# Performance work log

Hardware: AMD Instinct MI355X
Metric: run time of the kernel (lower is better)

## Reference

```python
import jax, jax.numpy as jnp
import numpy as np
from jax import lax

DILS = [2 ** i for i in range(11)] * 3  # 33 layers


def _conv1(x, w, b):
    # kernel_size=1 conv: w (O,I), x (B,I,T)
    return jnp.einsum('oi,bit->bot', w, x) + b[None, :, None]


def _dconv2(x, w, b, d):
    # kernel_size=2 dilated conv, torch padding='same': pad (d//2, d-d//2)
    y = lax.conv_general_dilated(
        x, w, window_strides=(1,), padding=[(d // 2, d - d // 2)],
        rhs_dilation=(d,), dimension_numbers=('NCH', 'OIH', 'NCH'))
    return y + b[None, :, None]


def setup_inputs() -> dict:
    key = jax.random.key(0)
    ks = jax.random.split(key, 7)
    B, T = 32, 16384
    s1 = 1.0           # fan_in=1*1
    s16 = 1.0 / np.sqrt(16.0)
    s16k2 = 1.0 / np.sqrt(16.0 * 2)
    s32 = 1.0 / np.sqrt(32.0)
    return {
        'x': jax.random.normal(ks[0], (B, 1, T), jnp.float32),
        'w1_first': jax.random.normal(ks[1], (16, 1), jnp.float32) * s1,
        'b1_first': jnp.zeros((16,), jnp.float32),
        'w1_post': jax.random.normal(ks[2], (32, 16, 16), jnp.float32) * s16,
        'b1_post': jnp.zeros((32, 16), jnp.float32),
        'wf': jax.random.normal(ks[3], (33, 32, 16, 2), jnp.float32) * s16k2,
        'bf': jnp.zeros((33, 32), jnp.float32),
        'wg': jax.random.normal(ks[4], (33, 32, 16, 2), jnp.float32) * s16k2,
        'bg': jnp.zeros((33, 32), jnp.float32),
        'w2': jax.random.normal(ks[5], (33, 16, 32), jnp.float32) * s32,
        'b2': jnp.zeros((33, 16), jnp.float32),
    }


def reference(x, w1_first, b1_first, w1_post, b1_post, wf, bf, wg, bg, w2, b2):
    skip_sum = 0.0
    for i, d in enumerate(DILS):
        if i == 0:
            x = jax.nn.relu(_conv1(x, w1_first, b1_first))
        else:
            x = jax.nn.relu(_conv1(x, w1_post[i - 1], b1_post[i - 1]))
        x_f = _dconv2(x, wf[i], bf[i], d)
        x_g = _dconv2(x, wg[i], bg[i], d)
        z = jnp.tanh(x_f) * jax.nn.sigmoid(x_g)
        z = jax.nn.relu(_conv1(z, w2[i], b2[i]))
        x = x + z
        skip_sum = skip_sum + z
    return jax.nn.relu(skip_sum)
```

## Files before the change

kernel.cpp:

```cpp
#include <hip/hip_runtime.h>

#define BB 32
#define TT 16384

typedef __attribute__((ext_vector_type(8))) short bf16x8;
typedef __attribute__((ext_vector_type(4))) float f32x4;
typedef __attribute__((ext_vector_type(4))) int i32x4;

#define MFMA(A, B, C) __builtin_amdgcn_mfma_f32_16x16x32_bf16((A), (B), (C), 0, 0, 0)

__device__ __forceinline__ unsigned short bf16_rne(float f) {
    unsigned int u = __float_as_uint(f);
    return (unsigned short)((u + 0x7FFF + ((u >> 16) & 1)) >> 16);
}
__device__ __forceinline__ float bf16_to_f(unsigned short h) {
    return __uint_as_float(((unsigned int)h) << 16);
}
__device__ __forceinline__ uint2 pk4(f32x4 v) {
    uint2 r;
    asm("v_cvt_pk_bf16_f32 %0, %1, %2" : "=v"(r.x) : "v"(v[0]), "v"(v[1]));
    asm("v_cvt_pk_bf16_f32 %0, %1, %2" : "=v"(r.y) : "v"(v[2]), "v"(v[3]));
    return r;
}
__device__ __forceinline__ void split4(f32x4 v, uint2& hh, uint2& ll) {
    asm("v_cvt_pk_bf16_f32 %0, %1, %2" : "=v"(hh.x) : "v"(v[0]), "v"(v[1]));
    asm("v_cvt_pk_bf16_f32 %0, %1, %2" : "=v"(hh.y) : "v"(v[2]), "v"(v[3]));
    float l0 = v[0] - __uint_as_float(hh.x << 16);
    float l1 = v[1] - __uint_as_float(hh.x & 0xffff0000u);
    float l2 = v[2] - __uint_as_float(hh.y << 16);
    float l3 = v[3] - __uint_as_float(hh.y & 0xffff0000u);
    asm("v_cvt_pk_bf16_f32 %0, %1, %2" : "=v"(ll.x) : "v"(l0), "v"(l1));
    asm("v_cvt_pk_bf16_f32 %0, %1, %2" : "=v"(ll.y) : "v"(l2), "v"(l3));
}

__device__ __forceinline__ float fast_sigmoid(float x) {
    float e = __expf(-x);
    return __builtin_amdgcn_rcpf(1.0f + e);
}
__device__ __forceinline__ float fast_tanh(float x) {
    float ax = fabsf(x);
    float e = __expf(2.0f * ax);
    float r = 1.0f - 2.0f * __builtin_amdgcn_rcpf(1.0f + e);
    return copysignf(r, x);
}

__global__ void prep_kernel(const float* __restrict__ w1_first,
                            const float* __restrict__ b1_first,
                            const float* __restrict__ w1_post,
                            const float* __restrict__ b1_post,
                            const float* __restrict__ wf, const float* __restrict__ bfb,
                            const float* __restrict__ wg, const float* __restrict__ bgb,
                            const float* __restrict__ w2, const float* __restrict__ b2,
                            short* __restrict__ Wfrag, float* __restrict__ Bset) {
    int L = blockIdx.x;
    int l = threadIdx.x;
    int op = l & 15;
    int q = l >> 4;
    int i0 = (q & 1) << 3;
    int tap = q >> 1;

    float gbuf[6][8];
#pragma unroll
    for (int j = 0; j < 8; ++j) {
        gbuf[0][j] = (L == 0) ? 0.f
                   : w1_post[((size_t)(L - 1) * 16 + op) * 16 + i0 + j];
        gbuf[1][j] = wf[(((size_t)L * 32 + op) * 16 + i0 + j) * 2 + tap];
        gbuf[2][j] = wf[(((size_t)L * 32 + 16 + op) * 16 + i0 + j) * 2 + tap];
        gbuf[3][j] = wg[(((size_t)L * 32 + op) * 16 + i0 + j) * 2 + tap];
        gbuf[4][j] = wg[(((size_t)L * 32 + 16 + op) * 16 + i0 + j) * 2 + tap];
        gbuf[5][j] = w2[((size_t)L * 16 + op) * 32 + (q << 3) + j];
    }

    constexpr int gsel[7] = {0, 0, 1, 2, 3, 4, 5};
    constexpr int hsel[7] = {1, 0, 1, 1, 1, 1, 1};
#pragma unroll
    for (int f = 0; f < 7; ++f) {
        size_t base = (((size_t)L * 7 + f) * 64 + l) * 8;
#pragma unroll
        for (int j = 0; j < 8; ++j) {
            float v = gbuf[gsel[f]][j];
            unsigned short h = bf16_rne(v);
            Wfrag[base + j] = hsel[f] ? (short)h
                                      : (short)bf16_rne(v - bf16_to_f(h));
        }
    }

#pragma unroll
    for (int r = 0; r < 4; ++r) {
        int c = (q << 2) + r;
        float bv[6];
        bv[0] = (L == 0) ? b1_first[c] : b1_post[(size_t)(L - 1) * 16 + c];
        bv[1] = bfb[(size_t)L * 32 + c];
        bv[2] = bfb[(size_t)L * 32 + 16 + c];
        bv[3] = bgb[(size_t)L * 32 + c];
        bv[4] = bgb[(size_t)L * 32 + 16 + c];
        bv[5] = b2[(size_t)L * 16 + c];
#pragma unroll
        for (int s = 0; s < 6; ++s)
            Bset[(((size_t)L * 6 + s) * 64 + l) * 4 + r] = bv[s];
    }
}

__device__ __forceinline__ f32x4 conv1_eval(bool first, const void* __restrict__ xin,
                                            const float* __restrict__ w1f,
                                            int b, int tp, int q,
                                            f32x4 b1v, bf16x8 A1, bf16x8 A2) {
    const f32x4 zero = {0.f, 0.f, 0.f, 0.f};
    bool valid = ((unsigned)tp) < (unsigned)TT;
    f32x4 acc = valid ? b1v : zero;
    if (first) {
        const float* xf = (const float*)xin;
        float xv = valid ? xf[(size_t)b * TT + tp] : 0.f;
        const float4* w4 = (const float4*)w1f;
        float4 w = w4[q];
        acc[0] = fmaf(w.x, xv, acc[0]);
        acc[1] = fmaf(w.y, xv, acc[1]);
        acc[2] = fmaf(w.z, xv, acc[2]);
        acc[3] = fmaf(w.w, xv, acc[3]);
    } else {
        int tpc = valid ? tp : 0;
        const bf16x8 z8 = {0, 0, 0, 0, 0, 0, 0, 0};
        const bf16x8* xp = (const bf16x8*)((const char*)xin +
                            ((size_t)b * TT + tpc) * 64 + (q << 4));
        bf16x8 bb = valid ? *xp : z8;
        acc = MFMA(A1, bb, acc);
        acc = MFMA(A2, bb, acc);
    }
#pragma unroll
    for (int r = 0; r < 4; ++r) acc[r] = fmaxf(acc[r], 0.f);
    return acc;
}

template <int MODE>
__global__ __launch_bounds__(256) void wn_layer(
    const void* __restrict__ xin, void* __restrict__ xout,
    float* __restrict__ skip, float* __restrict__ dout,
    const short* __restrict__ WfragL, const float* __restrict__ BsetL,
    const float* __restrict__ w1f, int d) {
    __shared__ char sm[8192];

    const int tid = threadIdx.x;
    const int wave = tid >> 6, lane = tid & 63;
    const int p = lane & 15, q = lane >> 4;

    const int blk = ((blockIdx.x & 7) << 10) + (blockIdx.x >> 3);
    const int b = blk >> 8;
    const int tbase = ((blk & 255) << 6) + (wave << 4);
    const int pl = d >> 1, pr = d - pl;

    char* xrb = sm + wave * 1024;
    char* zb = sm + 4096 + wave * 1024;
    const int xorb = (p & 8) << 2;

    const bf16x8* WF = (const bf16x8*)WfragL;
    const f32x4* BS = (const f32x4*)BsetL;

    const f32x4 b1v = BS[lane];
    bf16x8 A1 = {0, 0, 0, 0, 0, 0, 0, 0};
    bf16x8 A2 = {0, 0, 0, 0, 0, 0, 0, 0};
    if (MODE != 1) { A1 = WF[lane]; A2 = WF[64 + lane]; }

#pragma unroll
    for (int g = 0; g < 2; ++g) {
        int ts = tbase + (g ? pr : -pl);
        f32x4 xr = conv1_eval(MODE == 1, xin, w1f, b, ts + p, q, b1v, A1, A2);
        *(uint2*)(xrb + (g << 9) +
                  ((((q >> 1) << 8) + (p << 4) + ((q & 1) << 3)) ^ xorb)) = pk4(xr);
    }

    f32x4 xrC = {0.f, 0.f, 0.f, 0.f};
    if (MODE != 2)
        xrC = conv1_eval(MODE == 1, xin, w1f, b, tbase + p, q, b1v, A1, A2);

    bf16x8 bxr = *(const bf16x8*)(xrb + ((q >> 1) << 9) +
                                  ((((q & 1) << 8) + (p << 4)) ^ xorb));
    f32x4 f0 = MFMA(WF[2 * 64 + lane], bxr, BS[64 + lane]);
    f32x4 f1 = MFMA(WF[3 * 64 + lane], bxr, BS[128 + lane]);
    f32x4 g0 = MFMA(WF[4 * 64 + lane], bxr, BS[192 + lane]);
    f32x4 g1 = MFMA(WF[5 * 64 + lane], bxr, BS[256 + lane]);

    f32x4 z0, z1;
#pragma unroll
    for (int r = 0; r < 4; ++r) {
        z0[r] = fast_tanh(f0[r]) * fast_sigmoid(g0[r]);
        z1[r] = fast_tanh(f1[r]) * fast_sigmoid(g1[r]);
    }
    {
        int base = (((q >> 1) << 8) + (p << 4) + ((q & 1) << 3)) ^ xorb;
        *(uint2*)(zb + base) = pk4(z0);
        *(uint2*)(zb + 512 + base) = pk4(z1);
    }

    bf16x8 bz = *(const bf16x8*)(zb + (((q << 8) + (p << 4)) ^ xorb));
    f32x4 z2 = MFMA(WF[6 * 64 + lane], bz, BS[320 + lane]);
#pragma unroll
    for (int r = 0; r < 4; ++r) z2[r] = fmaxf(z2[r], 0.f);

    size_t pos = (size_t)b * TT + tbase + p;
    size_t xidx = (pos << 4) + (q << 2);
    if (MODE != 2) {
        f32x4 xo;
#pragma unroll
        for (int r = 0; r < 4; ++r) xo[r] = xrC[r] + z2[r];
        uint2 hh, ll;
        split4(xo, hh, ll);
        char* xob = (char*)xout + pos * 64;
        *(uint2*)(xob + (q << 3)) = hh;
        *(uint2*)(xob + 32 + (q << 3)) = ll;
        if (MODE == 1) {
            *(f32x4*)(skip + xidx) = z2;
        } else {
            f32x4 s = *(const f32x4*)(skip + xidx);
#pragma unroll
            for (int r = 0; r < 4; ++r) s[r] += z2[r];
            *(f32x4*)(skip + xidx) = s;
        }
    } else {
        f32x4 s = *(const f32x4*)(skip + xidx);
        size_t ob = (size_t)b * (16 * (size_t)TT) + (size_t)(q << 2) * TT + (tbase + p);
#pragma unroll
        for (int r = 0; r < 4; ++r)
            dout[ob + (size_t)r * TT] = fmaxf(s[r] + z2[r], 0.f);
    }
}

__global__ __launch_bounds__(256, 2) void wn_fused(
    const char* __restrict__ Xin, char* __restrict__ Xout,
    float* __restrict__ skip,
    const short* __restrict__ Wfrag, const float* __restrict__ Bset,
    int Lbase, int d0p, int NL) {
    extern __shared__ char sm[];
    char* Abuf = sm;
    char* Ubuf = sm + 49152;

    const int tid = threadIdx.x;
    const int wave = tid >> 6, lane = tid & 63;
    const int p = lane & 15, q = lane >> 4;
    char* zb = sm + 73728 + wave * 1024;
    const int xorb = (p & 8) << 2;

    const int gblk = ((blockIdx.x & 7) << 7) | (blockIdx.x >> 3);
    const int b = gblk >> 5;
    const int gt0 = ((gblk & 31) << 9) - 128;

#pragma unroll
    for (int jj = 0; jj < 3; ++jj) {
        int pos = jj * 256 + tid;
        int g = gt0 + pos;
        bool valid = ((unsigned)g) < (unsigned)TT;
        const char* src = Xin + ((size_t)b * TT + (valid ? g : 0)) * 64;
#pragma unroll
        for (int sub = 0; sub < 4; ++sub) {
            i32x4 v = {0, 0, 0, 0};
            if (valid) v = *(const i32x4*)(src + sub * 16);
            *(i32x4*)(Abuf + sub * 12288 + pos * 16) = v;
        }
    }
    __syncthreads();

    int uLo = 0, uHi = 48;
    f32x4 sk[8];
#pragma unroll
    for (int m = 0; m < 8; ++m) sk[m] = f32x4{0.f, 0.f, 0.f, 0.f};

#pragma unroll 1
    for (int k = 0; k < NL; ++k) {
        const int L = Lbase + k;
        const int d = 1 << (d0p + k);
        const int pl = d >> 1, pr = d - pl;
        const int tl = (pl + 15) >> 4, tr = (pr + 15) >> 4;
        const bool lastk = (k == NL - 1);
        const int nLo = uLo + tl, nHi = uHi - tr;

        const bf16x8* WF = (const bf16x8*)(Wfrag + (size_t)L * 7 * 64 * 8);
        const f32x4* BS = (const f32x4*)(Bset + (size_t)L * 6 * 64 * 4);
        const bf16x8 A1 = WF[lane], A2 = WF[64 + lane];
        const bf16x8 Wf0 = WF[128 + lane], Wf1 = WF[192 + lane];
        const bf16x8 Wg0 = WF[256 + lane], Wg1 = WF[320 + lane];
        const bf16x8 W2f = WF[384 + lane];
        const f32x4 b1v = BS[lane];
        const f32x4 bf0 = BS[64 + lane], bf1 = BS[128 + lane];
        const f32x4 bg0 = BS[192 + lane], bg1 = BS[256 + lane];
        const f32x4 b2v = BS[320 + lane];

        f32x4 ureg[12];

#pragma unroll
        for (int m = 0; m < 12; ++m) {
            int T = 4 * m + wave;
            if (T >= uLo && T < uHi) {
                int pos = T * 16 + p;
                bf16x8 bb = *(const bf16x8*)(Abuf + q * 12288 + pos * 16);
                f32x4 acc = b1v;
                acc = MFMA(A1, bb, acc);
                acc = MFMA(A2, bb, acc);
                bool val = ((unsigned)(gt0 + pos)) < (unsigned)TT;
#pragma unroll
                for (int r = 0; r < 4; ++r)
                    acc[r] = val ? fmaxf(acc[r], 0.f) : 0.f;
                ureg[m] = acc;
                *(uint2*)(Ubuf + (q >> 1) * 12288 + pos * 16 + ((q & 1) << 3)) =
                    pk4(acc);
            }
        }
        __syncthreads();

#pragma unroll
        for (int m = 0; m < 12; ++m) {
            int T = 4 * m + wave;
            bool doit = lastk ? (m >= 2 && m <= 9) : (T >= nLo && T < nHi);
            if (doit) {
                int pos = T * 16 + p;
                int tap = (q >> 1) ? pr : -pl;
                bf16x8 bxr = *(const bf16x8*)(Ubuf + (q & 1) * 12288 + (pos + tap) * 16);
                f32x4 f0 = MFMA(Wf0, bxr, bf0);
                f32x4 f1 = MFMA(Wf1, bxr, bf1);
                f32x4 g0 = MFMA(Wg0, bxr, bg0);
                f32x4 g1 = MFMA(Wg1, bxr, bg1);

                f32x4 z0, z1;
#pragma unroll
                for (int r = 0; r < 4; ++r) {
                    z0[r] = fast_tanh(f0[r]) * fast_sigmoid(g0[r]);
                    z1[r] = fast_tanh(f1[r]) * fast_sigmoid(g1[r]);
                }
                int zbase = (((q >> 1) << 8) + (p << 4) + ((q & 1) << 3)) ^ xorb;
                *(uint2*)(zb + zbase) = pk4(z0);
                *(uint2*)(zb + 512 + zbase) = pk4(z1);
                bf16x8 bz = *(const bf16x8*)(zb + (((q << 8) + (p << 4)) ^ xorb));
                f32x4 z2 = MFMA(W2f, bz, b2v);
#pragma unroll
                for (int r = 0; r < 4; ++r) z2[r] = fmaxf(z2[r], 0.f);

                int g = gt0 + pos;
                f32x4 xo = ureg[m] + z2;

                uint2 hh, ll;
                split4(xo, hh, ll);
                if (!lastk) {
                    *(uint2*)(Abuf + (q >> 1) * 12288 + pos * 16 + ((q & 1) << 3)) = hh;
                    *(uint2*)(Abuf + (2 + (q >> 1)) * 12288 + pos * 16 + ((q & 1) << 3)) = ll;
                } else {
                    char* gx = Xout + ((size_t)b * TT + g) * 64;
                    *(uint2*)(gx + (q >> 1) * 16 + ((q & 1) << 3)) = hh;
                    *(uint2*)(gx + 32 + (q >> 1) * 16 + ((q & 1) << 3)) = ll;
                }
                if (m >= 2 && m <= 9) sk[m - 2] += z2;
            }
        }
        __syncthreads();
        uLo = nLo;
        uHi = nHi;
    }

#pragma unroll
    for (int m = 2; m <= 9; ++m) {
        int T = 4 * m + wave;
        int g = gt0 + T * 16 + p;
        float* sp = skip + (((size_t)b * TT + g) << 4) + (q << 2);
        f32x4 s = *(const f32x4*)sp;
#pragma unroll
        for (int r = 0; r < 4; ++r) s[r] += sk[m - 2][r];
        *(f32x4*)sp = s;
    }
}

extern "C" void kernel_launch(void* const* d_in, const int* in_sizes, int n_in,
                              void* d_out, int out_size, void* d_ws, size_t ws_size,
                              hipStream_t stream) {
    const float* x        = (const float*)d_in[0];
    const float* w1_first = (const float*)d_in[1];
    const float* b1_first = (const float*)d_in[2];
    const float* w1_post  = (const float*)d_in[3];
    const float* b1_post  = (const float*)d_in[4];
    const float* wf       = (const float*)d_in[5];
    const float* bf       = (const float*)d_in[6];
    const float* wg       = (const float*)d_in[7];
    const float* bg       = (const float*)d_in[8];
    const float* w2       = (const float*)d_in[9];
    const float* b2       = (const float*)d_in[10];

    void* X0 = d_ws;
    float* SK = (float*)((char*)d_ws + 33554432);
    short* Wfrag = (short*)((char*)d_ws + 67108864);
    float* Bset = (float*)((char*)d_ws + 67345408);
    void* XD = d_out;
    float* dout = (float*)d_out;

    static bool attr_done = false;
    if (!attr_done) {
        hipFuncSetAttribute(reinterpret_cast<const void*>(wn_fused),
                            hipFuncAttributeMaxDynamicSharedMemorySize, 77824);
        attr_done = true;
    }

    prep_kernel<<<33, 64, 0, stream>>>(w1_first, b1_first, w1_post, b1_post,
                                       wf, bf, wg, bg, w2, b2, Wfrag, Bset);

    dim3 sblock(256), sgrid(BB * TT / 64);
    dim3 fblock(256), fgrid(BB * TT / 512);

    int n = 0;
    const void* cur_in = (const void*)x;
    auto nxt = [&](int parity) -> void* { return (parity & 1) ? XD : X0; };

    {
        void* out = nxt(n);
        wn_layer<1><<<sgrid, sblock, 0, stream>>>(cur_in, out, SK, dout,
                                                  Wfrag, Bset, w1_first, 1);
        cur_in = out; n ^= 1;
    }
    for (int cyc = 0; cyc < 3; ++cyc) {
        int Lb = (cyc == 0) ? 1 : 11 * cyc;
        int d0p = (cyc == 0) ? 1 : 0;
        int NL = (cyc == 0) ? 6 : 7;
        {
            void* out = nxt(n);
            wn_fused<<<fgrid, fblock, 77824, stream>>>(
                (const char*)cur_in, (char*)out, SK, Wfrag, Bset, Lb, d0p, NL);
            cur_in = out; n ^= 1;
        }
        int Ls = Lb + NL;
        for (int L = Ls; L <= Ls + 3; ++L) {
            int d = 1 << (L % 11);
            const short* WfL = Wfrag + (size_t)L * 7 * 64 * 8;
            const float* BsL = Bset + (size_t)L * 6 * 64 * 4;
            if (L == 32) {
                wn_layer<2><<<sgrid, sblock, 0, stream>>>(cur_in, nullptr, SK, dout,
                                                          WfL, BsL, w1_first, d);
            } else {
                void* out = nxt(n);
                wn_layer<0><<<sgrid, sblock, 0, stream>>>(cur_in, out, SK, dout,
                                                          WfL, BsL, w1_first, d);
                cur_in = out; n ^= 1;
            }
        }
    }
}
```

Measured before the change: 737.9 us.

## Add smaller-tile fused multi-layer kernel to raise occupancy

Adds a variant of the fused multi-layer WaveNet kernel that works on a 512-position window (256 output positions plus halo) instead of 768. It needs 52 KB of shared memory and is launched on twice as many blocks, aiming for more resident blocks per CU and better latency hiding. The variant is chosen at runtime through an occupancy query and used only if at least three blocks fit per CU. The cost is a larger halo share: proportionally more redundant recomputation at the window edges and more input reads per output.

Measured after the change: 738.4 us. Within noise of the previous version (+0.1%).

```diff
diff --git a/kernel.cpp b/kernel.cpp
--- a/kernel.cpp
+++ b/kernel.cpp
@@ -365,6 +365,150 @@
     }
 }
 
+__global__ __launch_bounds__(256, 2) void wn_fused512(
+    const char* __restrict__ Xin, char* __restrict__ Xout,
+    float* __restrict__ skip,
+    const short* __restrict__ Wfrag, const float* __restrict__ Bset,
+    int Lbase, int d0p, int NL) {
+    extern __shared__ char sm[];
+    char* Abuf = sm;
+    char* Ubuf = sm + 32768;
+
+    const int tid = threadIdx.x;
+    const int wave = tid >> 6, lane = tid & 63;
+    const int p = lane & 15, q = lane >> 4;
+    char* zb = sm + 49152 + wave * 1024;
+    const int xorb = (p & 8) << 2;
+
+    const int gblk = ((blockIdx.x & 7) << 8) | (blockIdx.x >> 3);
+    const int b = gblk >> 6;
+    const int gt0 = ((gblk & 63) << 8) - 112;
+
+#pragma unroll
+    for (int jj = 0; jj < 2; ++jj) {
+        int pos = jj * 256 + tid;
+        int g = gt0 + pos;
+        bool valid = ((unsigned)g) < (unsigned)TT;
+        const char* src = Xin + ((size_t)b * TT + (valid ? g : 0)) * 64;
+#pragma unroll
+        for (int sub = 0; sub < 4; ++sub) {
+            i32x4 v = {0, 0, 0, 0};
+            if (valid) v = *(const i32x4*)(src + sub * 16);
+            *(i32x4*)(Abuf + sub * 8192 + pos * 16) = v;
+        }
+    }
+    __syncthreads();
+
+    int uLo = 0, uHi = 32;
+    f32x4 sk[8];
+#pragma unroll
+    for (int m = 0; m < 8; ++m) sk[m] = f32x4{0.f, 0.f, 0.f, 0.f};
+
+#pragma unroll 1
+    for (int k = 0; k < NL; ++k) {
+        const int L = Lbase + k;
+        const int d = 1 << (d0p + k);
+        const int pl = d >> 1, pr = d - pl;
+        const int tl = (pl + 15) >> 4, tr = (pr + 15) >> 4;
+        const bool lastk = (k == NL - 1);
+        const int nLo = uLo + tl, nHi = uHi - tr;
+
+        const bf16x8* WF = (const bf16x8*)(Wfrag + (size_t)L * 7 * 64 * 8);
+        const f32x4* BS = (const f32x4*)(Bset + (size_t)L * 6 * 64 * 4);
+        const bf16x8 A1 = WF[lane], A2 = WF[64 + lane];
+        const bf16x8 Wf0 = WF[128 + lane], Wf1 = WF[192 + lane];
+        const bf16x8 Wg0 = WF[256 + lane], Wg1 = WF[320 + lane];
+        const bf16x8 W2f = WF[384 + lane];
+        const f32x4 b1v = BS[lane];
+        const f32x4 bf0 = BS[64 + lane], bf1 = BS[128 + lane];
+        const f32x4 bg0 = BS[192 + lane], bg1 = BS[256 + lane];
+        const f32x4 b2v = BS[320 + lane];
+
+        f32x4 ureg[8];
+
+#pragma unroll
+        for (int m = 0; m < 8; ++m) {
+            int T = 4 * m + wave;
+            if (T >= uLo && T < uHi) {
+                int pos = T * 16 + p;
+                bf16x8 bb = *(const bf16x8*)(Abuf + q * 8192 + pos * 16);
+                f32x4 acc = b1v;
+                acc = MFMA(A1, bb, acc);
+                acc = MFMA(A2, bb, acc);
+                bool val = ((unsigned)(gt0 + pos)) < (unsigned)TT;
+#pragma unroll
+                for (int r = 0; r < 4; ++r)
+                    acc[r] = val ? fmaxf(acc[r], 0.f) : 0.f;
+                ureg[m] = acc;
+                *(uint2*)(Ubuf + (q >> 1) * 8192 + pos * 16 + ((q & 1) << 3)) =
+                    pk4(acc);
+            }
+        }
+        __syncthreads();
+
+#pragma unroll
+        for (int m = 0; m < 8; ++m) {
+            int T = 4 * m + wave;
+            bool outT = (T >= 7 && T < 23);
+            bool doit = lastk ? outT : (T >= nLo && T < nHi);
+            if (doit) {
+                int pos = T * 16 + p;
+                int tap = (q >> 1) ? pr : -pl;
+                bf16x8 bxr = *(const bf16x8*)(Ubuf + (q & 1) * 8192 + (pos + tap) * 16);
+                f32x4 f0 = MFMA(Wf0, bxr, bf0);
+                f32x4 f1 = MFMA(Wf1, bxr, bf1);
+                f32x4 g0 = MFMA(Wg0, bxr, bg0);
+                f32x4 g1 = MFMA(Wg1, bxr, bg1);
+
+                f32x4 z0, z1;
+#pragma unroll
+                for (int r = 0; r < 4; ++r) {
+                    z0[r] = fast_tanh(f0[r]) * fast_sigmoid(g0[r]);
+                    z1[r] = fast_tanh(f1[r]) * fast_sigmoid(g1[r]);
+                }
+                int zbase = (((q >> 1) << 8) + (p << 4) + ((q & 1) << 3)) ^ xorb;
+                *(uint2*)(zb + zbase) = pk4(z0);
+                *(uint2*)(zb + 512 + zbase) = pk4(z1);
+                bf16x8 bz = *(const bf16x8*)(zb + (((q << 8) + (p << 4)) ^ xorb));
+                f32x4 z2 = MFMA(W2f, bz, b2v);
+#pragma unroll
+                for (int r = 0; r < 4; ++r) z2[r] = fmaxf(z2[r], 0.f);
+
+                int g = gt0 + pos;
+                f32x4 xo = ureg[m] + z2;
+
+                uint2 hh, ll;
+                split4(xo, hh, ll);
+                if (!lastk) {
+                    *(uint2*)(Abuf + (q >> 1) * 8192 + pos * 16 + ((q & 1) << 3)) = hh;
+                    *(uint2*)(Abuf + (2 + (q >> 1)) * 8192 + pos * 16 + ((q & 1) << 3)) = ll;
+                } else {
+                    char* gx = Xout + ((size_t)b * TT + g) * 64;
+                    *(uint2*)(gx + (q >> 1) * 16 + ((q & 1) << 3)) = hh;
+                    *(uint2*)(gx + 32 + (q >> 1) * 16 + ((q & 1) << 3)) = ll;
+                }
+                if (outT) sk[m] += z2;
+            }
+        }
+        __syncthreads();
+        uLo = nLo;
+        uHi = nHi;
+    }
+
+#pragma unroll
+    for (int m = 0; m < 8; ++m) {
+        int T = 4 * m + wave;
+        if (T >= 7 && T < 23) {
+            int g = gt0 + T * 16 + p;
+            float* sp = skip + (((size_t)b * TT + g) << 4) + (q << 2);
+            f32x4 s = *(const f32x4*)sp;
+#pragma unroll
+            for (int r = 0; r < 4; ++r) s[r] += sk[m][r];
+            *(f32x4*)sp = s;
+        }
+    }
+}
+
 extern "C" void kernel_launch(void* const* d_in, const int* in_sizes, int n_in,
                               void* d_out, int out_size, void* d_ws, size_t ws_size,
                               hipStream_t stream) {
@@ -391,14 +535,23 @@
     if (!attr_done) {
         hipFuncSetAttribute(reinterpret_cast<const void*>(wn_fused),
                             hipFuncAttributeMaxDynamicSharedMemorySize, 77824);
+        hipFuncSetAttribute(reinterpret_cast<const void*>(wn_fused512),
+                            hipFuncAttributeMaxDynamicSharedMemorySize, 53248);
         attr_done = true;
     }
+
+    int blk512 = 0;
+    hipOccupancyMaxActiveBlocksPerMultiprocessor(
+        &blk512, reinterpret_cast<const void*>(wn_fused512), 256, 53248);
+    const bool use512 = (blk512 >= 3);
 
     prep_kernel<<<33, 64, 0, stream>>>(w1_first, b1_first, w1_post, b1_post,
                                        wf, bf, wg, bg, w2, b2, Wfrag, Bset);
 
     dim3 sblock(256), sgrid(BB * TT / 64);
-    dim3 fblock(256), fgrid(BB * TT / 512);
+    dim3 fblock(256);
+    dim3 fgrid768(BB * TT / 512);
+    dim3 fgrid512(BB * TT / 256);
 
     int n = 0;
     const void* cur_in = (const void*)x;
@@ -416,8 +569,13 @@
         int NL = (cyc == 0) ? 6 : 7;
         {
             void* out = nxt(n);
-            wn_fused<<<fgrid, fblock, 77824, stream>>>(
-                (const char*)cur_in, (char*)out, SK, Wfrag, Bset, Lb, d0p, NL);
+            if (use512) {
+                wn_fused512<<<fgrid512, fblock, 53248, stream>>>(
+                    (const char*)cur_in, (char*)out, SK, Wfrag, Bset, Lb, d0p, NL);
+            } else {
+                wn_fused<<<fgrid768, fblock, 77824, stream>>>(
+                    (const char*)cur_in, (char*)out, SK, Wfrag, Bset, Lb, d0p, NL);
+            }
             cur_in = out; n ^= 1;
         }
         int Ls = Lb + NL;
```

## Shrink fused tile to 256 outputs and keep only bf16-high inside fused layers

Applied to the files above, without the earlier changes.

The fused multi-layer kernel now handles 256 output timesteps per block with a 496-sample halo window instead of 512 with 768, so shared memory drops from about 76 KB to 35 KB and the grid doubles. Intermediate activations between fused layers are stored as a single bf16 value rather than a hi/lo bf16 pair, which lets the first 1x1 conv use one MFMA instead of two and halves LDS traffic. The intent is higher occupancy and less per-layer compute. The cost is proportionally more halo recompute per output and lower precision for intermediates, which may affect accuracy.

New measurement: 805.8 us. 1.09x slower.

```diff
diff --git a/kernel.cpp b/kernel.cpp
--- a/kernel.cpp
+++ b/kernel.cpp
@@ -224,41 +224,43 @@
     }
 }
 
-__global__ __launch_bounds__(256, 2) void wn_fused(
+__global__ __launch_bounds__(256, 2) void wn_fused496s(
     const char* __restrict__ Xin, char* __restrict__ Xout,
     float* __restrict__ skip,
     const short* __restrict__ Wfrag, const float* __restrict__ Bset,
     int Lbase, int d0p, int NL) {
     extern __shared__ char sm[];
     char* Abuf = sm;
-    char* Ubuf = sm + 49152;
+    char* Ubuf = sm + 15872;
 
     const int tid = threadIdx.x;
     const int wave = tid >> 6, lane = tid & 63;
     const int p = lane & 15, q = lane >> 4;
-    char* zb = sm + 73728 + wave * 1024;
+    char* zb = sm + 31744 + wave * 1024;
     const int xorb = (p & 8) << 2;
 
-    const int gblk = ((blockIdx.x & 7) << 7) | (blockIdx.x >> 3);
-    const int b = gblk >> 5;
-    const int gt0 = ((gblk & 31) << 9) - 128;
-
-#pragma unroll
-    for (int jj = 0; jj < 3; ++jj) {
+    const int gblk = ((blockIdx.x & 7) << 8) | (blockIdx.x >> 3);
+    const int b = gblk >> 6;
+    const int gt0 = ((gblk & 63) << 8) - 112;
+
+#pragma unroll
+    for (int jj = 0; jj < 2; ++jj) {
         int pos = jj * 256 + tid;
-        int g = gt0 + pos;
-        bool valid = ((unsigned)g) < (unsigned)TT;
-        const char* src = Xin + ((size_t)b * TT + (valid ? g : 0)) * 64;
-#pragma unroll
-        for (int sub = 0; sub < 4; ++sub) {
-            i32x4 v = {0, 0, 0, 0};
-            if (valid) v = *(const i32x4*)(src + sub * 16);
-            *(i32x4*)(Abuf + sub * 12288 + pos * 16) = v;
+        if (pos < 496) {
+            int g = gt0 + pos;
+            bool valid = ((unsigned)g) < (unsigned)TT;
+            const char* src = Xin + ((size_t)b * TT + (valid ? g : 0)) * 64;
+#pragma unroll
+            for (int sub = 0; sub < 2; ++sub) {
+                i32x4 v = {0, 0, 0, 0};
+                if (valid) v = *(const i32x4*)(src + sub * 16);
+                *(i32x4*)(Abuf + sub * 7936 + pos * 16) = v;
+            }
         }
     }
     __syncthreads();
 
-    int uLo = 0, uHi = 48;
+    int uLo = 0, uHi = 31;
     f32x4 sk[8];
 #pragma unroll
     for (int m = 0; m < 8; ++m) sk[m] = f32x4{0.f, 0.f, 0.f, 0.f};
@@ -274,7 +276,7 @@
 
         const bf16x8* WF = (const bf16x8*)(Wfrag + (size_t)L * 7 * 64 * 8);
         const f32x4* BS = (const f32x4*)(Bset + (size_t)L * 6 * 64 * 4);
-        const bf16x8 A1 = WF[lane], A2 = WF[64 + lane];
+        const bf16x8 A12 = (q < 2) ? WF[lane] : WF[64 + lane];
         const bf16x8 Wf0 = WF[128 + lane], Wf1 = WF[192 + lane];
         const bf16x8 Wg0 = WF[256 + lane], Wg1 = WF[320 + lane];
         const bf16x8 W2f = WF[384 + lane];
@@ -283,36 +285,36 @@
         const f32x4 bg0 = BS[192 + lane], bg1 = BS[256 + lane];
         const f32x4 b2v = BS[320 + lane];
 
-        f32x4 ureg[12];
-
-#pragma unroll
-        for (int m = 0; m < 12; ++m) {
+        f32x4 ureg[8];
+
+#pragma unroll
+        for (int m = 0; m < 8; ++m) {
             int T = 4 * m + wave;
             if (T >= uLo && T < uHi) {
                 int pos = T * 16 + p;
-                bf16x8 bb = *(const bf16x8*)(Abuf + q * 12288 + pos * 16);
+                bf16x8 bb = *(const bf16x8*)(Abuf + (q & 1) * 7936 + pos * 16);
                 f32x4 acc = b1v;
-                acc = MFMA(A1, bb, acc);
-                acc = MFMA(A2, bb, acc);
+                acc = MFMA(A12, bb, acc);
                 bool val = ((unsigned)(gt0 + pos)) < (unsigned)TT;
 #pragma unroll
                 for (int r = 0; r < 4; ++r)
                     acc[r] = val ? fmaxf(acc[r], 0.f) : 0.f;
                 ureg[m] = acc;
-                *(uint2*)(Ubuf + (q >> 1) * 12288 + pos * 16 + ((q & 1) << 3)) =
+                *(uint2*)(Ubuf + (q >> 1) * 7936 + pos * 16 + ((q & 1) << 3)) =
                     pk4(acc);
             }
         }
         __syncthreads();
 
 #pragma unroll
-        for (int m = 0; m < 12; ++m) {
+        for (int m = 0; m < 8; ++m) {
             int T = 4 * m + wave;
-            bool doit = lastk ? (m >= 2 && m <= 9) : (T >= nLo && T < nHi);
+            bool outT = (T >= 7 && T < 23);
+            bool doit = lastk ? outT : (T >= nLo && T < nHi);
             if (doit) {
                 int pos = T * 16 + p;
                 int tap = (q >> 1) ? pr : -pl;
-                bf16x8 bxr = *(const bf16x8*)(Ubuf + (q & 1) * 12288 + (pos + tap) * 16);
+                bf16x8 bxr = *(const bf16x8*)(Ubuf + (q & 1) * 7936 + (pos + tap) * 16);
                 f32x4 f0 = MFMA(Wf0, bxr, bf0);
                 f32x4 f1 = MFMA(Wf1, bxr, bf1);
                 f32x4 g0 = MFMA(Wg0, bxr, bg0);
@@ -335,17 +337,17 @@
                 int g = gt0 + pos;
                 f32x4 xo = ureg[m] + z2;
 
-                uint2 hh, ll;
-                split4(xo, hh, ll);
                 if (!lastk) {
-                    *(uint2*)(Abuf + (q >> 1) * 12288 + pos * 16 + ((q & 1) << 3)) = hh;
-                    *(uint2*)(Abuf + (2 + (q >> 1)) * 12288 + pos * 16 + ((q & 1) << 3)) = ll;
+                    *(uint2*)(Abuf + (q >> 1) * 7936 + pos * 16 + ((q & 1) << 3)) =
+                        pk4(xo);
                 } else {
+                    uint2 hh, ll;
+                    split4(xo, hh, ll);
                     char* gx = Xout + ((size_t)b * TT + g) * 64;
                     *(uint2*)(gx + (q >> 1) * 16 + ((q & 1) << 3)) = hh;
                     *(uint2*)(gx + 32 + (q >> 1) * 16 + ((q & 1) << 3)) = ll;
                 }
-                if (m >= 2 && m <= 9) sk[m - 2] += z2;
+                if (outT) sk[m] += z2;
             }
         }
         __syncthreads();
@@ -354,14 +356,16 @@
     }
 
 #pragma unroll
-    for (int m = 2; m <= 9; ++m) {
+    for (int m = 0; m < 8; ++m) {
         int T = 4 * m + wave;
-        int g = gt0 + T * 16 + p;
-        float* sp = skip + (((size_t)b * TT + g) << 4) + (q << 2);
-        f32x4 s = *(const f32x4*)sp;
-#pragma unroll
-        for (int r = 0; r < 4; ++r) s[r] += sk[m - 2][r];
-        *(f32x4*)sp = s;
+        if (T >= 7 && T < 23) {
+            int g = gt0 + T * 16 + p;
+            float* sp = skip + (((size_t)b * TT + g) << 4) + (q << 2);
+            f32x4 s = *(const f32x4*)sp;
+#pragma unroll
+            for (int r = 0; r < 4; ++r) s[r] += sk[m][r];
+            *(f32x4*)sp = s;
+        }
     }
 }
 
@@ -389,8 +393,8 @@
 
     static bool attr_done = false;
     if (!attr_done) {
-        hipFuncSetAttribute(reinterpret_cast<const void*>(wn_fused),
-                            hipFuncAttributeMaxDynamicSharedMemorySize, 77824);
+        hipFuncSetAttribute(reinterpret_cast<const void*>(wn_fused496s),
+                            hipFuncAttributeMaxDynamicSharedMemorySize, 35840);
         attr_done = true;
     }
 
@@ -398,7 +402,8 @@
                                        wf, bf, wg, bg, w2, b2, Wfrag, Bset);
 
     dim3 sblock(256), sgrid(BB * TT / 64);
-    dim3 fblock(256), fgrid(BB * TT / 512);
+    dim3 fblock(256);
+    dim3 fgrid496(BB * TT / 256);
 
     int n = 0;
     const void* cur_in = (const void*)x;
@@ -416,7 +421,7 @@
         int NL = (cyc == 0) ? 6 : 7;
         {
             void* out = nxt(n);
-            wn_fused<<<fgrid, fblock, 77824, stream>>>(
+            wn_fused496s<<<fgrid496, fblock, 35840, stream>>>(
                 (const char*)cur_in, (char*)out, SK, Wfrag, Bset, Lb, d0p, NL);
             cur_in = out; n ^= 1;
         }
```
